# Kernel optimization log

Hardware: AMD Instinct MI355X
Metric: run time of the kernel (lower is better)

The kernel has to match this reference:

```python
import jax, jax.numpy as jnp
import numpy as np

B, S, D = 4, 1024, 2048
H = 4096
NE = 8
TOPK = 2


def setup_inputs() -> dict:
    key = jax.random.key(0)
    ks = jax.random.split(key, 9)
    s = lambda fan_in: 1.0 / np.sqrt(fan_in)
    return {
        "x": jax.random.normal(ks[0], (B, S, D), dtype=jnp.float32),
        "W1": jax.random.normal(ks[1], (NE, D, H), dtype=jnp.float32) * s(D),
        "b1": jnp.zeros((NE, H), dtype=jnp.float32),
        "W2": jax.random.normal(ks[2], (NE, H, H), dtype=jnp.float32) * s(H),
        "b2": jnp.zeros((NE, H), dtype=jnp.float32),
        "W3": jax.random.normal(ks[3], (NE, H, D), dtype=jnp.float32) * s(H),
        "b3": jnp.zeros((NE, D), dtype=jnp.float32),
        "Wg": jax.random.normal(ks[4], (D, NE), dtype=jnp.float32) * s(D),
        "bg": jnp.zeros((NE,), dtype=jnp.float32),
    }


def reference(x, W1, b1, W2, b2, W3, b3, Wg, bg):
    # Gating: softmax over experts, then top-k
    gate_logits = jnp.einsum("bsd,dn->bsn", x, Wg) + bg          # [B,S,NE]
    gate_weights = jax.nn.softmax(gate_logits, axis=-1)
    topv, topi = jax.lax.top_k(gate_weights, TOPK)               # [B,S,K]

    # Dense compute of ALL experts (faithful to original)
    h = jax.nn.gelu(jnp.einsum("bsd,ndh->nbsh", x, W1) + b1[:, None, None, :], approximate=False)
    h = jax.nn.gelu(jnp.einsum("nbsh,nhf->nbsf", h, W2) + b2[:, None, None, :], approximate=False)
    eo = jnp.einsum("nbsf,nfd->nbsd", h, W3) + b3[:, None, None, :]  # [NE,B,S,D]

    # Weighted combine of top-k experts per token via sparse one-hot weights
    comb = jnp.sum(jax.nn.one_hot(topi, NE, dtype=x.dtype) * topv[..., None], axis=-2)  # [B,S,NE]
    out = jnp.einsum("nbsd,bsn->bsd", eo, comb)
    return out
```

## Files before the change

kernel.cpp:

```cpp
#include <hip/hip_runtime.h>
#include <math.h>

#define NT 4096
#define Dm 2048
#define Hm 4096
#define NEx 8
#define CAPROWS 9216

typedef float f32x4 __attribute__((ext_vector_type(4)));
typedef _Float16 f16x8 __attribute__((ext_vector_type(8)));

__global__ void k_init(int* meta) {
    if (threadIdx.x < NEx) meta[threadIdx.x] = 0;
}

__global__ void k_gate(const float* __restrict__ x, const float* __restrict__ Wg,
                       const float* __restrict__ bg, int* __restrict__ meta,
                       int* __restrict__ list, float* __restrict__ topw) {
    int t = blockIdx.x;
    int lane = threadIdx.x;
    const float* xr = x + (size_t)t * Dm;
    double acc[NEx];
#pragma unroll
    for (int j = 0; j < NEx; ++j) acc[j] = 0.0;
    for (int d = lane; d < Dm; d += 64) {
        double xv = (double)xr[d];
        const float* wr = Wg + (size_t)d * NEx;
#pragma unroll
        for (int j = 0; j < NEx; ++j) acc[j] += xv * (double)wr[j];
    }
#pragma unroll
    for (int off = 32; off > 0; off >>= 1) {
#pragma unroll
        for (int j = 0; j < NEx; ++j) acc[j] += __shfl_xor(acc[j], off, 64);
    }
    if (lane == 0) {
        double l[NEx];
#pragma unroll
        for (int j = 0; j < NEx; ++j) l[j] = acc[j] + (double)bg[j];
        double m = l[0];
        for (int j = 1; j < NEx; ++j) m = l[j] > m ? l[j] : m;
        double s = 0.0, ev[NEx];
        for (int j = 0; j < NEx; ++j) { ev[j] = exp(l[j] - m); s += ev[j]; }
        int i0 = 0; double v0 = l[0];
        for (int j = 1; j < NEx; ++j) if (l[j] > v0) { v0 = l[j]; i0 = j; }
        int i1 = -1; double v1 = -1e300;
        for (int j = 0; j < NEx; ++j) if (j != i0 && l[j] > v1) { v1 = l[j]; i1 = j; }
        topw[2 * t]     = (float)(ev[i0] / s);
        topw[2 * t + 1] = (float)(ev[i1] / s);
        int p0 = atomicAdd(&meta[i0], 1); list[i0 * NT + p0] = 2 * t;
        int p1 = atomicAdd(&meta[i1], 1); list[i1 * NT + p1] = 2 * t + 1;
    }
}

__global__ void k_plan(int* meta) {
    if (threadIdx.x == 0 && blockIdx.x == 0) {
        int tot = 0;
        for (int e = 0; e < NEx; ++e) {
            int c = meta[e];
            meta[8 + e] = c;
            int cp = (c + 127) & ~127;
            meta[16 + e] = cp;
            meta[24 + e] = tot;
            tot += cp;
        }
        meta[32] = tot;
    }
}

__global__ void k_gather(const float* __restrict__ x, const int* __restrict__ meta,
                         const int* __restrict__ list, int* __restrict__ pos_of,
                         _Float16* __restrict__ Xg) {
    int r = blockIdx.x;
    if (r >= meta[32]) return;
    int e = 0;
    while (r >= meta[24 + e + 1]) ++e;
    int i = r - meta[24 + e];
    _Float16* dst = Xg + (size_t)r * Dm + threadIdx.x * 8;
    if (i < meta[8 + e]) {
        int v = list[e * NT + i];
        int t = v >> 1;
        if (threadIdx.x == 0) pos_of[v] = r;
        const float* src = x + (size_t)t * Dm + threadIdx.x * 8;
        f32x4 a = *(const f32x4*)(src);
        f32x4 b = *(const f32x4*)(src + 4);
        f16x8 o;
        o[0] = (_Float16)a[0]; o[1] = (_Float16)a[1]; o[2] = (_Float16)a[2]; o[3] = (_Float16)a[3];
        o[4] = (_Float16)b[0]; o[5] = (_Float16)b[1]; o[6] = (_Float16)b[2]; o[7] = (_Float16)b[3];
        *(f16x8*)dst = o;
    } else {
        f16x8 z = (f16x8)(_Float16)0.0f;
        *(f16x8*)dst = z;
    }
}

__global__ void k_convw(const float* __restrict__ src, _Float16* __restrict__ dst,
                        int K, int N) {
    __shared__ float tile[64][65];
    int n0 = blockIdx.x * 64, k0 = blockIdx.y * 64;
    size_t ebase = (size_t)blockIdx.z * (size_t)K * (size_t)N;
    const float* S = src + ebase;
    _Float16* Dd = dst + ebase;
    int tx = threadIdx.x & 15, ty = threadIdx.x >> 4;
#pragma unroll
    for (int p = 0; p < 4; ++p) {
        int kr = p * 16 + ty;
        f32x4 v = *(const f32x4*)(S + (size_t)(k0 + kr) * N + n0 + tx * 4);
        tile[kr][tx * 4 + 0] = v[0]; tile[kr][tx * 4 + 1] = v[1];
        tile[kr][tx * 4 + 2] = v[2]; tile[kr][tx * 4 + 3] = v[3];
    }
    __syncthreads();
    int n = threadIdx.x >> 2, seg = threadIdx.x & 3;
    f16x8 o0, o1;
#pragma unroll
    for (int j = 0; j < 8; ++j) o0[j] = (_Float16)tile[seg * 16 + j][n];
#pragma unroll
    for (int j = 0; j < 8; ++j) o1[j] = (_Float16)tile[seg * 16 + 8 + j][n];
    _Float16* dp = Dd + (size_t)(n0 + n) * K + k0 + seg * 16;
    *(f16x8*)dp = o0;
    *(f16x8*)(dp + 8) = o1;
}

__device__ __forceinline__ void gload16(const void* g, void* l) {
    __builtin_amdgcn_global_load_lds((__attribute__((address_space(1))) void*)(g),
                                     (__attribute__((address_space(3))) void*)(l),
                                     16, 0, 0);
}

__device__ __forceinline__ float gelu_f(float v) {
    return 0.5f * v * (1.0f + erff(v * 0.70710678118654752f));
}

template <int KDIM, int NDIM, bool GELU>
__global__ __launch_bounds__(256, 2)
void k_gemm(const _Float16* __restrict__ Abase, const _Float16* __restrict__ Wt,
            const float* __restrict__ bias, void* __restrict__ Cout,
            const int* __restrict__ meta) {
    const int e = blockIdx.z;
    const int cp = meta[16 + e];
    const int mt = blockIdx.y;
    if (mt * 128 >= cp) return;
    const int nt = blockIdx.x;
    const int row0 = meta[24 + e] + mt * 128;

    __shared__ _Float16 ldsA[128 * 64];
    __shared__ _Float16 ldsB[128 * 64];

    const int tid = threadIdx.x;
    const int lane = tid & 63;
    const int wv = tid >> 6;
    const int wm = wv >> 1, wn = wv & 1;

    const char* Ag = (const char*)(Abase + (size_t)row0 * KDIM);
    const char* Bg = (const char*)(Wt + ((size_t)e * NDIM + (size_t)nt * 128) * KDIM);

    int soff[4];
#pragma unroll
    for (int r = 0; r < 4; ++r) {
        int L = r * 4096 + tid * 16;
        int row = L >> 7;
        int col = L & 127;
        int scol = col ^ ((row & 7) << 4);
        soff[r] = row * (KDIM * 2) + scol;
    }

    f32x4 acc[4][4];
#pragma unroll
    for (int i = 0; i < 4; ++i)
#pragma unroll
        for (int j = 0; j < 4; ++j)
            acc[i][j] = (f32x4){0.f, 0.f, 0.f, 0.f};

    int abase[4], aswz[4], bbase[4], bswz[4];
#pragma unroll
    for (int m = 0; m < 4; ++m) {
        int rA = wm * 64 + m * 16 + (lane & 15);
        abase[m] = rA * 128;
        aswz[m] = (rA & 7) << 4;
    }
#pragma unroll
    for (int n = 0; n < 4; ++n) {
        int rB = wn * 64 + n * 16 + (lane & 15);
        bbase[n] = rB * 128;
        bswz[n] = (rB & 7) << 4;
    }
    const int hib = (lane >> 4) * 16;

    const char* cldsA = (const char*)ldsA;
    const char* cldsB = (const char*)ldsB;

    for (int kt = 0; kt < KDIM / 64; ++kt) {
        const int kbyte = kt * 128;
#pragma unroll
        for (int r = 0; r < 4; ++r) {
            gload16(Ag + (soff[r] + kbyte), (char*)ldsA + r * 4096 + tid * 16);
            gload16(Bg + (soff[r] + kbyte), (char*)ldsB + r * 4096 + tid * 16);
        }
        __syncthreads();
#pragma unroll
        for (int ks = 0; ks < 2; ++ks) {
            const int cbs = ks * 64 + hib;
            f16x8 av[4], bv[4];
#pragma unroll
            for (int m = 0; m < 4; ++m)
                av[m] = *(const f16x8*)(cldsA + abase[m] + (cbs ^ aswz[m]));
#pragma unroll
            for (int n = 0; n < 4; ++n)
                bv[n] = *(const f16x8*)(cldsB + bbase[n] + (cbs ^ bswz[n]));
#pragma unroll
            for (int m = 0; m < 4; ++m)
#pragma unroll
                for (int n = 0; n < 4; ++n)
                    acc[m][n] = __builtin_amdgcn_mfma_f32_16x16x32_f16(av[m], bv[n], acc[m][n], 0, 0, 0);
        }
        __syncthreads();
    }

    const int lcol = lane & 15;
    const int rowq = (lane >> 4) * 4;
#pragma unroll
    for (int m = 0; m < 4; ++m) {
#pragma unroll
        for (int n = 0; n < 4; ++n) {
            const int gcol = nt * 128 + wn * 64 + n * 16 + lcol;
            const float bb = bias[(size_t)e * NDIM + gcol];
#pragma unroll
            for (int v = 0; v < 4; ++v) {
                const int grow = row0 + wm * 64 + m * 16 + rowq + v;
                float val = acc[m][n][v] + bb;
                if constexpr (GELU) {
                    ((_Float16*)Cout)[(size_t)grow * NDIM + gcol] = (_Float16)gelu_f(val);
                } else {
                    ((float*)Cout)[(size_t)grow * NDIM + gcol] = val;
                }
            }
        }
    }
}

__global__ void k_combine(const float* __restrict__ eo, const int* __restrict__ pos_of,
                          const float* __restrict__ topw, float* __restrict__ out) {
    int t = blockIdx.x;
    int r0 = pos_of[2 * t], r1 = pos_of[2 * t + 1];
    float w0 = topw[2 * t], w1 = topw[2 * t + 1];
    const f32x4* e0 = (const f32x4*)(eo + (size_t)r0 * Dm);
    const f32x4* e1 = (const f32x4*)(eo + (size_t)r1 * Dm);
    f32x4* op = (f32x4*)(out + (size_t)t * Dm);
    for (int i = threadIdx.x; i < Dm / 4; i += 256) {
        f32x4 a = e0[i], b = e1[i];
        op[i] = a * w0 + b * w1;
    }
}

extern "C" void kernel_launch(void* const* d_in, const int* in_sizes, int n_in,
                              void* d_out, int out_size, void* d_ws, size_t ws_size,
                              hipStream_t stream) {
    const float* x  = (const float*)d_in[0];
    const float* W1 = (const float*)d_in[1];
    const float* b1 = (const float*)d_in[2];
    const float* W2 = (const float*)d_in[3];
    const float* b2 = (const float*)d_in[4];
    const float* W3 = (const float*)d_in[5];
    const float* b3 = (const float*)d_in[6];
    const float* Wg = (const float*)d_in[7];
    const float* bg = (const float*)d_in[8];
    float* out = (float*)d_out;
    (void)in_sizes; (void)n_in; (void)out_size; (void)ws_size;

    char* ws = (char*)d_ws;
    int*   meta   = (int*)ws;
    int*   list   = (int*)(ws + 256);
    int*   pos_of = (int*)(ws + 256 + 131072);
    float* topw   = (float*)(ws + 256 + 131072 + 32768);
    size_t off = 196864;
    _Float16* Xg = (_Float16*)(ws + off); off += (size_t)CAPROWS * Dm * 2;
    _Float16* Wb = (_Float16*)(ws + off); off += (size_t)NEx * Hm * Hm * 2;
    _Float16* h2 = (_Float16*)(ws + off); off += (size_t)CAPROWS * Hm * 2;
    _Float16* h1 = (_Float16*)(ws + off);
    float*    eo = (float*)(ws + off);

    k_init<<<1, 64, 0, stream>>>(meta);
    k_gate<<<NT, 64, 0, stream>>>(x, Wg, bg, meta, list, topw);
    k_plan<<<1, 1, 0, stream>>>(meta);
    k_gather<<<CAPROWS, 256, 0, stream>>>(x, meta, list, pos_of, Xg);

    k_convw<<<dim3(Hm / 64, Dm / 64, NEx), 256, 0, stream>>>(W1, Wb, Dm, Hm);
    k_gemm<Dm, Hm, true><<<dim3(Hm / 128, 32, NEx), 256, 0, stream>>>(Xg, Wb, b1, (void*)h1, meta);

    k_convw<<<dim3(Hm / 64, Hm / 64, NEx), 256, 0, stream>>>(W2, Wb, Hm, Hm);
    k_gemm<Hm, Hm, true><<<dim3(Hm / 128, 32, NEx), 256, 0, stream>>>(h1, Wb, b2, (void*)h2, meta);

    k_convw<<<dim3(Dm / 64, Hm / 64, NEx), 256, 0, stream>>>(W3, Wb, Hm, Dm);
    k_gemm<Hm, Dm, false><<<dim3(Dm / 128, 32, NEx), 256, 0, stream>>>(h2, Wb, b3, (void*)eo, meta);

    k_combine<<<NT, 256, 0, stream>>>(eo, pos_of, topw, out);
}
```

Before: 1.158 ms.

## Use 256x256 double-buffered GEMM tiles with 512 threads and grid swizzle

The expert GEMM moves from 128x128 tiles with 256 threads and a single LDS buffer to 256x256 tiles with 8 waves. Two LDS stages are prefetched via global_load_lds with explicit vmcnt waits, and MFMA sections raise wave priority. Block indices are remapped so that concurrently running blocks share B tiles. Expert row padding goes to 256, which increases capacity rows and wasted compute on padding, and occupancy drops to one 128KB-LDS block per CU.

```diff
diff --git a/kernel.cpp b/kernel.cpp
--- a/kernel.cpp
+++ b/kernel.cpp
@@ -5,7 +5,7 @@
 #define Dm 2048
 #define Hm 4096
 #define NEx 8
-#define CAPROWS 9216
+#define CAPROWS 10240
 
 typedef float f32x4 __attribute__((ext_vector_type(4)));
 typedef _Float16 f16x8 __attribute__((ext_vector_type(8)));
@@ -59,7 +59,7 @@
         for (int e = 0; e < NEx; ++e) {
             int c = meta[e];
             meta[8 + e] = c;
-            int cp = (c + 127) & ~127;
+            int cp = (c + 255) & ~255;
             meta[16 + e] = cp;
             meta[24 + e] = tot;
             tot += cp;
@@ -127,106 +127,142 @@
                                      16, 0, 0);
 }
 
+__device__ __forceinline__ void bar() {
+    __builtin_amdgcn_sched_barrier(0);
+    asm volatile("" ::: "memory");
+    __builtin_amdgcn_s_barrier();
+    asm volatile("" ::: "memory");
+    __builtin_amdgcn_sched_barrier(0);
+}
+
 __device__ __forceinline__ float gelu_f(float v) {
     return 0.5f * v * (1.0f + erff(v * 0.70710678118654752f));
 }
 
 template <int KDIM, int NDIM, bool GELU>
-__global__ __launch_bounds__(256, 2)
+__global__ __launch_bounds__(512, 1)
 void k_gemm(const _Float16* __restrict__ Abase, const _Float16* __restrict__ Wt,
             const float* __restrict__ bias, void* __restrict__ Cout,
             const int* __restrict__ meta) {
+    constexpr int GX = NDIM / 256;
+    constexpr int GY = 32;
+    constexpr int NBLK = GX * GY;
+    constexpr int NKT = KDIM / 64;
+
     const int e = blockIdx.z;
     const int cp = meta[16 + e];
-    const int mt = blockIdx.y;
-    if (mt * 128 >= cp) return;
-    const int nt = blockIdx.x;
-    const int row0 = meta[24 + e] + mt * 128;
-
-    __shared__ _Float16 ldsA[128 * 64];
-    __shared__ _Float16 ldsB[128 * 64];
+    const int f = blockIdx.y * GX + blockIdx.x;
+    const int fp = (f & 7) * (NBLK >> 3) + (f >> 3);
+    const int nt = fp / GY;
+    const int mt = fp % GY;
+    if (mt * 256 >= cp) return;
+    const int row0 = meta[24 + e] + mt * 256;
+
+    __shared__ _Float16 lds[4][256 * 64];
 
     const int tid = threadIdx.x;
     const int lane = tid & 63;
     const int wv = tid >> 6;
-    const int wm = wv >> 1, wn = wv & 1;
+    const int wm = wv >> 2;
+    const int wn = wv & 3;
 
     const char* Ag = (const char*)(Abase + (size_t)row0 * KDIM);
-    const char* Bg = (const char*)(Wt + ((size_t)e * NDIM + (size_t)nt * 128) * KDIM);
-
-    int soff[4];
+    const char* Bg = (const char*)(Wt + ((size_t)e * NDIM + (size_t)nt * 256) * KDIM);
+
+    int gsoff[4], ldst[4];
 #pragma unroll
     for (int r = 0; r < 4; ++r) {
-        int L = r * 4096 + tid * 16;
-        int row = L >> 7;
-        int col = L & 127;
+        int row = (tid >> 3) + r * 64;
+        int col = (tid & 7) * 16;
         int scol = col ^ ((row & 7) << 4);
-        soff[r] = row * (KDIM * 2) + scol;
-    }
-
-    f32x4 acc[4][4];
-#pragma unroll
-    for (int i = 0; i < 4; ++i)
+        gsoff[r] = row * (KDIM * 2) + scol;
+        ldst[r] = r * 8192 + tid * 16;
+    }
+
+    auto STAGE = [&](int kt_, int p_) {
+        const int kb = kt_ * 128;
+#pragma unroll
+        for (int r = 0; r < 4; ++r)
+            gload16(Ag + gsoff[r] + kb, (char*)lds[p_ * 2] + ldst[r]);
+#pragma unroll
+        for (int r = 0; r < 4; ++r)
+            gload16(Bg + gsoff[r] + kb, (char*)lds[p_ * 2 + 1] + ldst[r]);
+    };
+
+    f32x4 acc[8][4];
+#pragma unroll
+    for (int i = 0; i < 8; ++i)
 #pragma unroll
         for (int j = 0; j < 4; ++j)
             acc[i][j] = (f32x4){0.f, 0.f, 0.f, 0.f};
 
-    int abase[4], aswz[4], bbase[4], bswz[4];
-#pragma unroll
-    for (int m = 0; m < 4; ++m) {
-        int rA = wm * 64 + m * 16 + (lane & 15);
-        abase[m] = rA * 128;
-        aswz[m] = (rA & 7) << 4;
-    }
+    const int l15 = lane & 15;
+    const int swzr = (lane & 7) << 4;
+    const int hib = (lane >> 4) * 16;
+    const int c0 = hib ^ swzr;
+    const int c1 = (64 + hib) ^ swzr;
+    int aoff[8], boff[4];
+#pragma unroll
+    for (int m = 0; m < 8; ++m) aoff[m] = (wm * 128 + m * 16 + l15) * 128;
+#pragma unroll
+    for (int n = 0; n < 4; ++n) boff[n] = (wn * 64 + n * 16 + l15) * 128;
+
+    STAGE(0, 0);
+    STAGE(1, 1);
+    asm volatile("s_waitcnt vmcnt(8)" ::: "memory");
+    bar();
+
+    for (int kt = 0; kt < NKT; ++kt) {
+        const int p = kt & 1;
+        const char* LA = (const char*)lds[p * 2];
+        const char* LB = (const char*)lds[p * 2 + 1];
+
+        f16x8 bv[4][2];
+#pragma unroll
+        for (int n = 0; n < 4; ++n) {
+            bv[n][0] = *(const f16x8*)(LB + boff[n] + c0);
+            bv[n][1] = *(const f16x8*)(LB + boff[n] + c1);
+        }
+#pragma unroll
+        for (int mh = 0; mh < 2; ++mh) {
+            f16x8 av[4][2];
+#pragma unroll
+            for (int i = 0; i < 4; ++i) {
+                av[i][0] = *(const f16x8*)(LA + aoff[mh * 4 + i] + c0);
+                av[i][1] = *(const f16x8*)(LA + aoff[mh * 4 + i] + c1);
+            }
+            __builtin_amdgcn_s_setprio(1);
+#pragma unroll
+            for (int i = 0; i < 4; ++i)
+#pragma unroll
+                for (int n = 0; n < 4; ++n) {
+                    acc[mh * 4 + i][n] = __builtin_amdgcn_mfma_f32_16x16x32_f16(av[i][0], bv[n][0], acc[mh * 4 + i][n], 0, 0, 0);
+                    acc[mh * 4 + i][n] = __builtin_amdgcn_mfma_f32_16x16x32_f16(av[i][1], bv[n][1], acc[mh * 4 + i][n], 0, 0, 0);
+                }
+            __builtin_amdgcn_s_setprio(0);
+        }
+
+        bar();
+        if (kt + 2 < NKT) {
+            STAGE(kt + 2, p);
+            asm volatile("s_waitcnt vmcnt(8)" ::: "memory");
+            bar();
+        } else if (kt + 1 < NKT) {
+            asm volatile("s_waitcnt vmcnt(0)" ::: "memory");
+            bar();
+        }
+    }
+
+    const int rowq = (lane >> 4) * 4;
 #pragma unroll
     for (int n = 0; n < 4; ++n) {
-        int rB = wn * 64 + n * 16 + (lane & 15);
-        bbase[n] = rB * 128;
-        bswz[n] = (rB & 7) << 4;
-    }
-    const int hib = (lane >> 4) * 16;
-
-    const char* cldsA = (const char*)ldsA;
-    const char* cldsB = (const char*)ldsB;
-
-    for (int kt = 0; kt < KDIM / 64; ++kt) {
-        const int kbyte = kt * 128;
-#pragma unroll
-        for (int r = 0; r < 4; ++r) {
-            gload16(Ag + (soff[r] + kbyte), (char*)ldsA + r * 4096 + tid * 16);
-            gload16(Bg + (soff[r] + kbyte), (char*)ldsB + r * 4096 + tid * 16);
-        }
-        __syncthreads();
-#pragma unroll
-        for (int ks = 0; ks < 2; ++ks) {
-            const int cbs = ks * 64 + hib;
-            f16x8 av[4], bv[4];
-#pragma unroll
-            for (int m = 0; m < 4; ++m)
-                av[m] = *(const f16x8*)(cldsA + abase[m] + (cbs ^ aswz[m]));
-#pragma unroll
-            for (int n = 0; n < 4; ++n)
-                bv[n] = *(const f16x8*)(cldsB + bbase[n] + (cbs ^ bswz[n]));
-#pragma unroll
-            for (int m = 0; m < 4; ++m)
-#pragma unroll
-                for (int n = 0; n < 4; ++n)
-                    acc[m][n] = __builtin_amdgcn_mfma_f32_16x16x32_f16(av[m], bv[n], acc[m][n], 0, 0, 0);
-        }
-        __syncthreads();
-    }
-
-    const int lcol = lane & 15;
-    const int rowq = (lane >> 4) * 4;
-#pragma unroll
-    for (int m = 0; m < 4; ++m) {
-#pragma unroll
-        for (int n = 0; n < 4; ++n) {
-            const int gcol = nt * 128 + wn * 64 + n * 16 + lcol;
-            const float bb = bias[(size_t)e * NDIM + gcol];
+        const int gcol = nt * 256 + wn * 64 + n * 16 + l15;
+        const float bb = bias[(size_t)e * NDIM + gcol];
+#pragma unroll
+        for (int m = 0; m < 8; ++m) {
 #pragma unroll
             for (int v = 0; v < 4; ++v) {
-                const int grow = row0 + wm * 64 + m * 16 + rowq + v;
+                const int grow = row0 + wm * 128 + m * 16 + rowq + v;
                 float val = acc[m][n][v] + bb;
                 if constexpr (GELU) {
                     ((_Float16*)Cout)[(size_t)grow * NDIM + gcol] = (_Float16)gelu_f(val);
@@ -285,13 +321,13 @@
     k_gather<<<CAPROWS, 256, 0, stream>>>(x, meta, list, pos_of, Xg);
 
     k_convw<<<dim3(Hm / 64, Dm / 64, NEx), 256, 0, stream>>>(W1, Wb, Dm, Hm);
-    k_gemm<Dm, Hm, true><<<dim3(Hm / 128, 32, NEx), 256, 0, stream>>>(Xg, Wb, b1, (void*)h1, meta);
+    k_gemm<Dm, Hm, true><<<dim3(Hm / 256, 32, NEx), 512, 0, stream>>>(Xg, Wb, b1, (void*)h1, meta);
 
     k_convw<<<dim3(Hm / 64, Hm / 64, NEx), 256, 0, stream>>>(W2, Wb, Hm, Hm);
-    k_gemm<Hm, Hm, true><<<dim3(Hm / 128, 32, NEx), 256, 0, stream>>>(h1, Wb, b2, (void*)h2, meta);
+    k_gemm<Hm, Hm, true><<<dim3(Hm / 256, 32, NEx), 512, 0, stream>>>(h1, Wb, b2, (void*)h2, meta);
 
     k_convw<<<dim3(Dm / 64, Hm / 64, NEx), 256, 0, stream>>>(W3, Wb, Hm, Dm);
-    k_gemm<Hm, Dm, false><<<dim3(Dm / 128, 32, NEx), 256, 0, stream>>>(h2, Wb, b3, (void*)eo, meta);
+    k_gemm<Hm, Dm, false><<<dim3(Dm / 256, 32, NEx), 512, 0, stream>>>(h2, Wb, b3, (void*)eo, meta);
 
     k_combine<<<NT, 256, 0, stream>>>(eo, pos_of, topw, out);
 }
```

Result: slower. 1.580 ms (+36.5%).

## Overlap weight fp16 conversion with gating and preceding GEMMs in fused launches

Applied to the files above, without the earlier changes.

Weight conversion tiles for the next layer are appended as extra blocks to the gating kernel and the previous GEMM launch, so the conversions run alongside compute instead of as separate serialized kernels. This needs separate buffers for each layer's converted weights, and a fallback path keeps the old serialized schedule when the workspace is too small. The gating kernel now packs four tokens per 256-thread block, and GEMM blocks are remapped from a flattened grid with a swizzle to change the cache access order. Under memory-bandwidth contention, conversion blocks may slow the concurrent GEMM blocks.

```diff
diff --git a/kernel.cpp b/kernel.cpp
--- a/kernel.cpp
+++ b/kernel.cpp
@@ -14,11 +14,56 @@
     if (threadIdx.x < NEx) meta[threadIdx.x] = 0;
 }
 
-__global__ void k_gate(const float* __restrict__ x, const float* __restrict__ Wg,
-                       const float* __restrict__ bg, int* __restrict__ meta,
-                       int* __restrict__ list, float* __restrict__ topw) {
-    int t = blockIdx.x;
-    int lane = threadIdx.x;
+__device__ __forceinline__ void conv_tile(const float* __restrict__ src, _Float16* __restrict__ dst,
+                                          int K, int N, int t, float (*tile)[65]) {
+    int nx = N >> 6, nk = K >> 6;
+    int nb = t % nx;
+    int kb = (t / nx) % nk;
+    int e  = t / (nx * nk);
+    int n0 = nb * 64, k0 = kb * 64;
+    size_t ebase = (size_t)e * (size_t)K * (size_t)N;
+    const float* S = src + ebase;
+    _Float16* Dd = dst + ebase;
+    int tx = threadIdx.x & 15, ty = threadIdx.x >> 4;
+#pragma unroll
+    for (int p = 0; p < 4; ++p) {
+        int kr = p * 16 + ty;
+        f32x4 v = *(const f32x4*)(S + (size_t)(k0 + kr) * N + n0 + tx * 4);
+        tile[kr][tx * 4 + 0] = v[0]; tile[kr][tx * 4 + 1] = v[1];
+        tile[kr][tx * 4 + 2] = v[2]; tile[kr][tx * 4 + 3] = v[3];
+    }
+    __syncthreads();
+    int n = threadIdx.x >> 2, seg = threadIdx.x & 3;
+    f16x8 o0, o1;
+#pragma unroll
+    for (int j = 0; j < 8; ++j) o0[j] = (_Float16)tile[seg * 16 + j][n];
+#pragma unroll
+    for (int j = 0; j < 8; ++j) o1[j] = (_Float16)tile[seg * 16 + 8 + j][n];
+    _Float16* dp = Dd + (size_t)(n0 + n) * K + k0 + seg * 16;
+    *(f16x8*)dp = o0;
+    *(f16x8*)(dp + 8) = o1;
+}
+
+__global__ __launch_bounds__(256, 2) void k_convw(const float* __restrict__ src,
+                                                  _Float16* __restrict__ dst, int K, int N) {
+    __shared__ float tile[64][65];
+    conv_tile(src, dst, K, N, blockIdx.x, tile);
+}
+
+__global__ __launch_bounds__(256, 2)
+void k_gateconv(const float* __restrict__ x, const float* __restrict__ Wg,
+                const float* __restrict__ bg, int* __restrict__ meta,
+                int* __restrict__ list, float* __restrict__ topw,
+                const float* __restrict__ csrc, _Float16* __restrict__ cdst,
+                int cK, int cN) {
+    __shared__ float tile[64][65];
+    const int bid = blockIdx.x;
+    if (bid >= NT / 4) {
+        conv_tile(csrc, cdst, cK, cN, bid - NT / 4, tile);
+        return;
+    }
+    int lane = threadIdx.x & 63;
+    int t = bid * 4 + (threadIdx.x >> 6);
     const float* xr = x + (size_t)t * Dm;
     double acc[NEx];
 #pragma unroll
@@ -94,33 +139,6 @@
     }
 }
 
-__global__ void k_convw(const float* __restrict__ src, _Float16* __restrict__ dst,
-                        int K, int N) {
-    __shared__ float tile[64][65];
-    int n0 = blockIdx.x * 64, k0 = blockIdx.y * 64;
-    size_t ebase = (size_t)blockIdx.z * (size_t)K * (size_t)N;
-    const float* S = src + ebase;
-    _Float16* Dd = dst + ebase;
-    int tx = threadIdx.x & 15, ty = threadIdx.x >> 4;
-#pragma unroll
-    for (int p = 0; p < 4; ++p) {
-        int kr = p * 16 + ty;
-        f32x4 v = *(const f32x4*)(S + (size_t)(k0 + kr) * N + n0 + tx * 4);
-        tile[kr][tx * 4 + 0] = v[0]; tile[kr][tx * 4 + 1] = v[1];
-        tile[kr][tx * 4 + 2] = v[2]; tile[kr][tx * 4 + 3] = v[3];
-    }
-    __syncthreads();
-    int n = threadIdx.x >> 2, seg = threadIdx.x & 3;
-    f16x8 o0, o1;
-#pragma unroll
-    for (int j = 0; j < 8; ++j) o0[j] = (_Float16)tile[seg * 16 + j][n];
-#pragma unroll
-    for (int j = 0; j < 8; ++j) o1[j] = (_Float16)tile[seg * 16 + 8 + j][n];
-    _Float16* dp = Dd + (size_t)(n0 + n) * K + k0 + seg * 16;
-    *(f16x8*)dp = o0;
-    *(f16x8*)(dp + 8) = o1;
-}
-
 __device__ __forceinline__ void gload16(const void* g, void* l) {
     __builtin_amdgcn_global_load_lds((__attribute__((address_space(1))) void*)(g),
                                      (__attribute__((address_space(3))) void*)(l),
@@ -133,18 +151,32 @@
 
 template <int KDIM, int NDIM, bool GELU>
 __global__ __launch_bounds__(256, 2)
-void k_gemm(const _Float16* __restrict__ Abase, const _Float16* __restrict__ Wt,
-            const float* __restrict__ bias, void* __restrict__ Cout,
-            const int* __restrict__ meta) {
-    const int e = blockIdx.z;
+void k_gemmconv(const _Float16* __restrict__ Abase, const _Float16* __restrict__ Wt,
+                const float* __restrict__ bias, void* __restrict__ Cout,
+                const int* __restrict__ meta,
+                const float* __restrict__ csrc, _Float16* __restrict__ cdst,
+                int cK, int cN, int nGemm) {
+    __shared__ char smem[32768];
+    const int bid = blockIdx.x;
+    if (bid >= nGemm) {
+        conv_tile(csrc, cdst, cK, cN, bid - nGemm, (float(*)[65])smem);
+        return;
+    }
+
+    constexpr int GX = NDIM / 128;
+    constexpr int GY = 32;
+    constexpr int NBLK = GX * GY;
+    const int e = bid / NBLK;
+    const int f = bid % NBLK;
+    const int fp = (f & 7) * (NBLK >> 3) + (f >> 3);
+    const int nt = fp / GY;
+    const int mt = fp % GY;
     const int cp = meta[16 + e];
-    const int mt = blockIdx.y;
     if (mt * 128 >= cp) return;
-    const int nt = blockIdx.x;
     const int row0 = meta[24 + e] + mt * 128;
 
-    __shared__ _Float16 ldsA[128 * 64];
-    __shared__ _Float16 ldsB[128 * 64];
+    _Float16* ldsA = (_Float16*)smem;
+    _Float16* ldsB = (_Float16*)(smem + 16384);
 
     const int tid = threadIdx.x;
     const int lane = tid & 63;
@@ -265,7 +297,7 @@
     const float* Wg = (const float*)d_in[7];
     const float* bg = (const float*)d_in[8];
     float* out = (float*)d_out;
-    (void)in_sizes; (void)n_in; (void)out_size; (void)ws_size;
+    (void)in_sizes; (void)n_in; (void)out_size;
 
     char* ws = (char*)d_ws;
     int*   meta   = (int*)ws;
@@ -273,25 +305,69 @@
     int*   pos_of = (int*)(ws + 256 + 131072);
     float* topw   = (float*)(ws + 256 + 131072 + 32768);
     size_t off = 196864;
-    _Float16* Xg = (_Float16*)(ws + off); off += (size_t)CAPROWS * Dm * 2;
-    _Float16* Wb = (_Float16*)(ws + off); off += (size_t)NEx * Hm * Hm * 2;
-    _Float16* h2 = (_Float16*)(ws + off); off += (size_t)CAPROWS * Hm * 2;
-    _Float16* h1 = (_Float16*)(ws + off);
-    float*    eo = (float*)(ws + off);
-
-    k_init<<<1, 64, 0, stream>>>(meta);
-    k_gate<<<NT, 64, 0, stream>>>(x, Wg, bg, meta, list, topw);
-    k_plan<<<1, 1, 0, stream>>>(meta);
-    k_gather<<<CAPROWS, 256, 0, stream>>>(x, meta, list, pos_of, Xg);
-
-    k_convw<<<dim3(Hm / 64, Dm / 64, NEx), 256, 0, stream>>>(W1, Wb, Dm, Hm);
-    k_gemm<Dm, Hm, true><<<dim3(Hm / 128, 32, NEx), 256, 0, stream>>>(Xg, Wb, b1, (void*)h1, meta);
-
-    k_convw<<<dim3(Hm / 64, Hm / 64, NEx), 256, 0, stream>>>(W2, Wb, Hm, Hm);
-    k_gemm<Hm, Hm, true><<<dim3(Hm / 128, 32, NEx), 256, 0, stream>>>(h1, Wb, b2, (void*)h2, meta);
-
-    k_convw<<<dim3(Dm / 64, Hm / 64, NEx), 256, 0, stream>>>(W3, Wb, Hm, Dm);
-    k_gemm<Hm, Dm, false><<<dim3(Dm / 128, 32, NEx), 256, 0, stream>>>(h2, Wb, b3, (void*)eo, meta);
-
-    k_combine<<<NT, 256, 0, stream>>>(eo, pos_of, topw, out);
-}
+
+    const int nC1 = (Hm / 64) * (Dm / 64) * NEx;
+    const int nC2 = (Hm / 64) * (Hm / 64) * NEx;
+    const int nC3 = (Dm / 64) * (Hm / 64) * NEx;
+    const int nG12 = NEx * (Hm / 128) * 32;
+    const int nG3  = NEx * (Dm / 128) * 32;
+
+    const size_t sXg  = (size_t)CAPROWS * Dm * 2;
+    const size_t sWb1 = (size_t)NEx * Dm * Hm * 2;
+    const size_t sWb2 = (size_t)NEx * Hm * Hm * 2;
+    const size_t sWb3 = (size_t)NEx * Hm * Dm * 2;
+    const size_t sH   = (size_t)CAPROWS * Hm * 2;
+
+    const size_t needPar = off + sXg + sWb1 + sWb2 + sWb3 + sH + sH;
+
+    if (ws_size >= needPar) {
+        _Float16* Xg  = (_Float16*)(ws + off); off += sXg;
+        _Float16* Wb1 = (_Float16*)(ws + off); off += sWb1;
+        _Float16* Wb2 = (_Float16*)(ws + off); off += sWb2;
+        _Float16* Wb3 = (_Float16*)(ws + off); off += sWb3;
+        _Float16* h1  = (_Float16*)(ws + off); off += sH;
+        _Float16* h2  = (_Float16*)(ws + off); off += sH;
+        float*    eo  = (float*)Wb1;
+
+        k_init<<<1, 64, 0, stream>>>(meta);
+        k_gateconv<<<NT / 4 + nC1, 256, 0, stream>>>(x, Wg, bg, meta, list, topw,
+                                                     W1, Wb1, Dm, Hm);
+        k_plan<<<1, 1, 0, stream>>>(meta);
+        k_gather<<<CAPROWS, 256, 0, stream>>>(x, meta, list, pos_of, Xg);
+
+        k_gemmconv<Dm, Hm, true><<<nG12 + nC2, 256, 0, stream>>>(
+            Xg, Wb1, b1, (void*)h1, meta, W2, Wb2, Hm, Hm, nG12);
+        k_gemmconv<Hm, Hm, true><<<nG12 + nC3, 256, 0, stream>>>(
+            h1, Wb2, b2, (void*)h2, meta, W3, Wb3, Hm, Dm, nG12);
+        k_gemmconv<Hm, Dm, false><<<nG3, 256, 0, stream>>>(
+            h2, Wb3, b3, (void*)eo, meta, (const float*)0, (_Float16*)0, 0, 0, nG3);
+
+        k_combine<<<NT, 256, 0, stream>>>(eo, pos_of, topw, out);
+    } else {
+        _Float16* Xg = (_Float16*)(ws + off); off += sXg;
+        _Float16* Wb = (_Float16*)(ws + off); off += sWb2;
+        _Float16* h2 = (_Float16*)(ws + off); off += sH;
+        _Float16* h1 = (_Float16*)(ws + off);
+        float*    eo = (float*)(ws + off);
+
+        k_init<<<1, 64, 0, stream>>>(meta);
+        k_gateconv<<<NT / 4, 256, 0, stream>>>(x, Wg, bg, meta, list, topw,
+                                               (const float*)0, (_Float16*)0, 0, 0);
+        k_plan<<<1, 1, 0, stream>>>(meta);
+        k_gather<<<CAPROWS, 256, 0, stream>>>(x, meta, list, pos_of, Xg);
+
+        k_convw<<<nC1, 256, 0, stream>>>(W1, Wb, Dm, Hm);
+        k_gemmconv<Dm, Hm, true><<<nG12, 256, 0, stream>>>(
+            Xg, Wb, b1, (void*)h1, meta, (const float*)0, (_Float16*)0, 0, 0, nG12);
+
+        k_convw<<<nC2, 256, 0, stream>>>(W2, Wb, Hm, Hm);
+        k_gemmconv<Hm, Hm, true><<<nG12, 256, 0, stream>>>(
+            h1, Wb, b2, (void*)h2, meta, (const float*)0, (_Float16*)0, 0, 0, nG12);
+
+        k_convw<<<nC3, 256, 0, stream>>>(W3, Wb, Hm, Dm);
+        k_gemmconv<Hm, Dm, false><<<nG3, 256, 0, stream>>>(
+            h2, Wb, b3, (void*)eo, meta, (const float*)0, (_Float16*)0, 0, 0, nG3);
+
+        k_combine<<<NT, 256, 0, stream>>>(eo, pos_of, topw, out);
+    }
+}
```

New measurement: 1.098 ms. -5.1%, faster.
